# Kernel optimization log

Measured on AMD Instinct MI355X. Metric: run time of the kernel, lower is better.

The kernel has to match this reference:

```python
import jax, jax.numpy as jnp
import numpy as np

N_NODES = 100000
N_EDGES = 6400000
N_TYPES = 16
A1, A2, A3 = 5e-06, 0.0005, 1e-08


def setup_inputs() -> dict:
    key = jax.random.key(0)
    k1, k2, k3, k4, k5, k6 = jax.random.split(key, 6)
    pos = jax.random.normal(k1, (N_NODES, 2), dtype=jnp.float32)
    vel = jax.random.normal(k2, (N_NODES, 2), dtype=jnp.float32)
    p_table = jax.random.uniform(k3, (N_TYPES, 3), dtype=jnp.float32, minval=0.5, maxval=2.0)
    field = jnp.ones((N_NODES, 1), dtype=jnp.float32)
    particle_type = jax.random.randint(k4, (N_NODES,), 0, N_TYPES, dtype=jnp.int32)
    # edges without self-loops (remove_self_loops already applied)
    dst = jax.random.randint(k5, (N_EDGES,), 0, N_NODES, dtype=jnp.int32)
    off = jax.random.randint(k6, (N_EDGES,), 1, N_NODES, dtype=jnp.int32)
    src = (dst + off) % N_NODES
    edge_index = jnp.stack([dst, src], axis=0)  # [2, E], row0=dst(i), row1=src(j)
    return {"pos": pos, "vel": vel, "p_table": p_table, "field": field,
            "particle_type": particle_type, "edge_index": edge_index}


def reference(pos, vel, p_table, field, particle_type, edge_index):
    dst = edge_index[0]  # receiver i
    src = edge_index[1]  # sender j
    dp = pos[src] - pos[dst]            # bc_dpos(pos_j - pos_i), identity BC  [E,2]
    dv = vel[src] - vel[dst]            # d_pos_j - d_pos_i                   [E,2]
    params = p_table[particle_type[dst]]  # parameters_i                      [E,3]
    d2 = jnp.sum(dp * dp, axis=1, keepdims=True)  # [E,1]
    safe_d2 = jnp.where(d2 > 0, d2, 1.0)
    cohesion = params[:, 0:1] * A1 * dp
    alignment = params[:, 1:2] * A2 * dv
    separation = -params[:, 2:3] * A3 * dp / safe_d2
    msg = (separation + alignment + cohesion) * field[src]  # [E,2]
    dd_pos = jax.ops.segment_sum(msg, dst, num_segments=pos.shape[0])  # [N,2]
    return dd_pos
```

## Files before the change

### kernel.cpp

```cpp
#include <hip/hip_runtime.h>
#include <hip/hip_fp16.h>


#define BA1 5e-06f
#define BA2 0.0005f
#define BA3 1e-08f

#define NT 256
#define NTS 1024
#define NWAVE 4
#define SEPB 8192
#define WIN 256
#define WSH 8
#define SPLIT 8
#define NBMAX 512
#define CAP 28672u
#define FPS 4194304.f

__global__ void __launch_bounds__(NT)
k_pack(const float* __restrict__ pos, const float* __restrict__ vel,
       const float* __restrict__ field,
       int N, int NB, int PBLK,
       float4* __restrict__ rec16, unsigned* __restrict__ cursor) {
    int bx = blockIdx.x, tid = threadIdx.x;
    if (bx == PBLK) {
        for (int b = tid; b < NB; b += NT) cursor[b] = (unsigned)b * CAP;
        return;
    }
    int i = bx * NT + tid;
    if (i >= N) return;
    float2 p = *reinterpret_cast<const float2*>(pos + 2 * i);
    float2 v = *reinterpret_cast<const float2*>(vel + 2 * i);
    unsigned short sx = __half_as_ushort(__float2half(v.x));
    unsigned short sy = __half_as_ushort(__float2half(v.y));
    unsigned pv = (unsigned)sx | ((unsigned)sy << 16);
    rec16[i] = make_float4(p.x, p.y, __uint_as_float(pv), field[i]);
}

__global__ void __launch_bounds__(NTS)
k_scatter(const int* __restrict__ dst, const int* __restrict__ src,
          int E, int NB,
          unsigned* __restrict__ cursor,
          unsigned* __restrict__ pk) {
    __shared__ unsigned lh[NBMAX];
    __shared__ unsigned lofs[NBMAX];
    __shared__ unsigned lcur[NBMAX];
    __shared__ unsigned gbase[NBMAX];
    __shared__ unsigned sbuf[SEPB];
    __shared__ unsigned short sbkt[SEPB];
    int blk = blockIdx.x, tid = threadIdx.x;
    int s = blk * SEPB, e = min(E, s + SEPB);

    for (int b = tid; b < NBMAX; b += NTS) lh[b] = 0u;
    __syncthreads();

    int k = s + 4 * tid;
    for (; k + 3 < e; k += 4 * NTS) {
        int4 d = *reinterpret_cast<const int4*>(dst + k);
        atomicAdd(&lh[d.x >> WSH], 1u);
        atomicAdd(&lh[d.y >> WSH], 1u);
        atomicAdd(&lh[d.z >> WSH], 1u);
        atomicAdd(&lh[d.w >> WSH], 1u);
    }
    {
        int rem = (e - s) & 3;
        if (tid < rem) atomicAdd(&lh[dst[e - rem + tid] >> WSH], 1u);
    }
    __syncthreads();
    for (int b = tid; b < NBMAX; b += NTS) lofs[b] = lh[b];
    __syncthreads();

    for (int o = 1; o < NBMAX; o <<= 1) {
        unsigned v0 = 0u, v1 = 0u;
        if (tid < 256) {
            v0 = (tid >= o) ? lh[tid - o] : 0u;
            v1 = (tid + 256 >= o) ? lh[tid + 256 - o] : 0u;
        }
        __syncthreads();
        if (tid < 256) {
            lh[tid] += v0;
            lh[tid + 256] += v1;
        }
        __syncthreads();
    }
    for (int b = tid; b < NBMAX; b += NTS) {
        unsigned c = lofs[b];
        unsigned ex = lh[b] - c;
        lofs[b] = ex;
        lcur[b] = ex;
        if (b < NB && c > 0u) gbase[b] = atomicAdd(&cursor[b], c);
    }
    __syncthreads();

    k = s + 4 * tid;
    for (; k + 3 < e; k += 4 * NTS) {
        int4 d = *reinterpret_cast<const int4*>(dst + k);
        int4 j = *reinterpret_cast<const int4*>(src + k);
        int b0 = d.x >> WSH; unsigned r0 = atomicAdd(&lcur[b0], 1u);
        sbuf[r0] = ((unsigned)(d.x & (WIN - 1)) << 24) | (unsigned)j.x; sbkt[r0] = (unsigned short)b0;
        int b1 = d.y >> WSH; unsigned r1 = atomicAdd(&lcur[b1], 1u);
        sbuf[r1] = ((unsigned)(d.y & (WIN - 1)) << 24) | (unsigned)j.y; sbkt[r1] = (unsigned short)b1;
        int b2 = d.z >> WSH; unsigned r2 = atomicAdd(&lcur[b2], 1u);
        sbuf[r2] = ((unsigned)(d.z & (WIN - 1)) << 24) | (unsigned)j.z; sbkt[r2] = (unsigned short)b2;
        int b3 = d.w >> WSH; unsigned r3 = atomicAdd(&lcur[b3], 1u);
        sbuf[r3] = ((unsigned)(d.w & (WIN - 1)) << 24) | (unsigned)j.w; sbkt[r3] = (unsigned short)b3;
    }
    {
        int rem = (e - s) & 3;
        if (tid < rem) {
            int kk = e - rem + tid;
            int d = dst[kk];
            int b = d >> WSH; unsigned r = atomicAdd(&lcur[b], 1u);
            sbuf[r] = ((unsigned)(d & (WIN - 1)) << 24) | (unsigned)src[kk]; sbkt[r] = (unsigned short)b;
        }
    }
    __syncthreads();

    int ne = e - s;
    for (int t = tid; t < ne; t += NTS) {
        unsigned b = sbkt[t];
        unsigned idx = gbase[b] + ((unsigned)t - lofs[b]);
        if (idx < (b + 1u) * CAP)
            pk[idx] = sbuf[t];
    }
}

__global__ void __launch_bounds__(NT, 4)
k_accum(const float4* __restrict__ rec16,
        const float* __restrict__ p_table,
        const int* __restrict__ ptype,
        const unsigned* __restrict__ pk,
        const unsigned* __restrict__ cursor,
        int N,
        float* __restrict__ out) {
    __shared__ float4 wnode[WIN];
    __shared__ float4 wcoef[WIN];
    __shared__ unsigned long long acc64[NWAVE][WIN];
    int b = blockIdx.x, tid = threadIdx.x;
    int bb = b << WSH;
    int wn = min(N - bb, WIN);
    int wv = tid >> 6;

    if (tid < wn) {
        int g = bb + tid;
        float4 r = rec16[g];
        unsigned u = __float_as_uint(r.z);
        float vx = __half2float(__ushort_as_half((unsigned short)(u & 0xFFFFu)));
        float vy = __half2float(__ushort_as_half((unsigned short)(u >> 16)));
        wnode[tid] = make_float4(r.x, r.y, vx, vy);
        int ty = ptype[g];
        wcoef[tid] = make_float4(p_table[3 * ty + 0] * BA1,
                                 p_table[3 * ty + 1] * BA2,
                                 p_table[3 * ty + 2] * BA3, 0.f);
    }
    {
        unsigned long long* a = &acc64[0][0];
        for (int t = tid; t < NWAVE * WIN; t += NT) a[t] = 0ull;
    }
    __syncthreads();

    unsigned s = (unsigned)b * CAP;
    unsigned c = cursor[b] - s;
    c = (c > CAP) ? CAP : c;
    unsigned e = s + c;

#define EDGE1(PV)                                                              \
    {                                                                          \
        unsigned p_ = (PV);                                                    \
        int l_ = (int)(p_ >> 24);                                              \
        int j_ = (int)(p_ & 0xFFFFFFu);                                        \
        float4 nj_ = rec16[j_];                                                \
        unsigned u_ = __float_as_uint(nj_.z);                                  \
        float vjx_ = __half2float(__ushort_as_half((unsigned short)(u_ & 0xFFFFu))); \
        float vjy_ = __half2float(__ushort_as_half((unsigned short)(u_ >> 16))); \
        float4 w_ = wnode[l_];                                                 \
        float4 c_ = wcoef[l_];                                                 \
        float dpx_ = nj_.x - w_.x, dpy_ = nj_.y - w_.y;                        \
        float dvx_ = vjx_ - w_.z, dvy_ = vjy_ - w_.w;                          \
        float d2_ = dpx_ * dpx_ + dpy_ * dpy_;                                 \
        float sd2_ = (d2_ > 0.f) ? d2_ : 1.f;                                  \
        float cdp_ = c_.x - c_.z / sd2_;                                       \
        float mx_ = (cdp_ * dpx_ + c_.y * dvx_) * nj_.w;                       \
        float my_ = (cdp_ * dpy_ + c_.y * dvy_) * nj_.w;                       \
        long long ax_ = (long long)(int)(mx_ * FPS);                           \
        long long ay_ = (long long)(int)(my_ * FPS);                           \
        atomicAdd(&acc64[wv][l_], (unsigned long long)((ax_ << 32) + ay_));    \
    }

    unsigned stride = (unsigned)NT * SPLIT * 4u;
    for (unsigned k0 = s + ((unsigned)blockIdx.y * NT + tid) * 4u;
         k0 + 4u <= e; k0 += stride) {
        uint4 a = *reinterpret_cast<const uint4*>(pk + k0);
        EDGE1(a.x); EDGE1(a.y); EDGE1(a.z); EDGE1(a.w);
    }
    unsigned tail = c & 3u;
    if (blockIdx.y == 0 && tid < (int)tail) EDGE1(pk[e - tail + tid]);
#undef EDGE1

    __syncthreads();
    for (int l = tid; l < wn; l += NT) {
        unsigned long long T = acc64[0][l] + acc64[1][l] +
                               acc64[2][l] + acc64[3][l];
        long long Ts = (long long)T;
        int yb = (int)(unsigned)(T & 0xFFFFFFFFull);
        long long rem = Ts - (long long)yb;
        int xb = (int)(rem >> 32);
        atomicAdd(&out[2 * (bb + l) + 0], (float)xb * (1.f / FPS));
        atomicAdd(&out[2 * (bb + l) + 1], (float)yb * (1.f / FPS));
    }
}

__global__ void boids_edge_kernel(const float* __restrict__ pos,
                                  const float* __restrict__ vel,
                                  const float* __restrict__ p_table,
                                  const float* __restrict__ field,
                                  const int* __restrict__ ptype,
                                  const int* __restrict__ dst_idx,
                                  const int* __restrict__ src_idx,
                                  float* __restrict__ out,
                                  int n_edges) {
    int e = blockIdx.x * blockDim.x + threadIdx.x;
    if (e >= n_edges) return;
    int i = dst_idx[e], j = src_idx[e];
    float2 pi = *reinterpret_cast<const float2*>(pos + 2 * i);
    float2 pj = *reinterpret_cast<const float2*>(pos + 2 * j);
    float2 vi = *reinterpret_cast<const float2*>(vel + 2 * i);
    float2 vj = *reinterpret_cast<const float2*>(vel + 2 * j);
    float dpx = pj.x - pi.x, dpy = pj.y - pi.y;
    float dvx = vj.x - vi.x, dvy = vj.y - vi.y;
    int t = ptype[i];
    float p0 = p_table[3 * t + 0], p1 = p_table[3 * t + 1], p2 = p_table[3 * t + 2];
    float d2 = dpx * dpx + dpy * dpy;
    float sd2 = (d2 > 0.0f) ? d2 : 1.0f;
    float cdp = p0 * BA1 - p2 * BA3 / sd2;
    float cdv = p1 * BA2;
    float f = field[j];
    atomicAdd(&out[2 * i + 0], (cdp * dpx + cdv * dvx) * f);
    atomicAdd(&out[2 * i + 1], (cdp * dpy + cdv * dvy) * f);
}

extern "C" void kernel_launch(void* const* d_in, const int* in_sizes, int n_in,
                              void* d_out, int out_size, void* d_ws, size_t ws_size,
                              hipStream_t stream) {
    const float* pos     = (const float*)d_in[0];
    const float* vel     = (const float*)d_in[1];
    const float* p_table = (const float*)d_in[2];
    const float* field   = (const float*)d_in[3];
    const int*   ptype   = (const int*)d_in[4];
    const int*   eidx    = (const int*)d_in[5];

    int N = in_sizes[0] / 2;
    int E = in_sizes[5] / 2;
    const int* dstI = eidx;
    const int* srcI = eidx + E;
    float* out = (float*)d_out;

    int NB    = (N + WIN - 1) >> WSH;
    int NSBLK = (E + SEPB - 1) / SEPB;
    int PBLK  = (N + NT - 1) / NT;

    size_t off_rec = 0;
    size_t off_pk  = off_rec + (size_t)N * sizeof(float4);
    size_t off_cur = off_pk + (size_t)NB * CAP * 4;
    size_t need    = off_cur + (size_t)NB * 4;

    bool ok = (ws_size >= need) && (NB <= NBMAX) && (N <= (1 << 24)) &&
              ((E & 3) == 0) &&
              ((size_t)(E / (NB > 0 ? NB : 1)) * 3 / 2 + 64 <= CAP);

    if (!ok) {
        hipMemsetAsync(out, 0, (size_t)out_size * sizeof(float), stream);
        int grid = (E + NT - 1) / NT;
        boids_edge_kernel<<<grid, NT, 0, stream>>>(pos, vel, p_table, field,
                                                   ptype, dstI, srcI, out, E);
        return;
    }

    float4*   rec16  = (float4*)((char*)d_ws + off_rec);
    unsigned* pk     = (unsigned*)((char*)d_ws + off_pk);
    unsigned* cursor = (unsigned*)((char*)d_ws + off_cur);

    hipMemsetAsync(out, 0, (size_t)out_size * sizeof(float), stream);

    k_pack   <<<PBLK + 1, NT, 0, stream>>>(pos, vel, field, N, NB, PBLK,
                                           rec16, cursor);
    k_scatter<<<NSBLK, NTS, 0, stream>>>(dstI, srcI, E, NB, cursor, pk);
    dim3 agrid(NB, SPLIT);
    k_accum  <<<agrid, NT, 0, stream>>>(rec16, p_table, ptype, pk, cursor,
                                        N, out);
}
```

Before: 79.88 us.

## Double destination window to 512 nodes and simplify bucket scatter scan

Destination windows grow from 256 to 512 nodes, which halves the bucket count to 196 and gives each accumulation block about twice as many edges. The local-index field in the packed edge word grows to 9 bits, leaving 23 bits for the source index. The scatter kernel processes larger chunks, drops the separate offset array by folding the exclusive offset into the global base, and uses byte-sized bucket tags to save LDS. The accumulate kernel raises its occupancy hint to 5, but its shared accumulators also double. Fewer, larger blocks may reduce per-block overhead and global cursor atomics, at the cost of lower parallelism and more LDS per block.

```diff
diff --git a/kernel.cpp b/kernel.cpp
--- a/kernel.cpp
+++ b/kernel.cpp
@@ -9,12 +9,12 @@
 #define NT 256
 #define NTS 1024
 #define NWAVE 4
-#define SEPB 8192
-#define WIN 256
-#define WSH 8
-#define SPLIT 8
-#define NBMAX 512
-#define CAP 28672u
+#define SEPB 12288
+#define WIN 512
+#define WSH 9
+#define SPLIT 16
+#define NBMAX 256
+#define CAP 49152u
 #define FPS 4194304.f
 
 __global__ void __launch_bounds__(NT)
@@ -43,15 +43,14 @@
           unsigned* __restrict__ cursor,
           unsigned* __restrict__ pk) {
     __shared__ unsigned lh[NBMAX];
-    __shared__ unsigned lofs[NBMAX];
     __shared__ unsigned lcur[NBMAX];
     __shared__ unsigned gbase[NBMAX];
     __shared__ unsigned sbuf[SEPB];
-    __shared__ unsigned short sbkt[SEPB];
+    __shared__ unsigned char sbkt[SEPB];
     int blk = blockIdx.x, tid = threadIdx.x;
     int s = blk * SEPB, e = min(E, s + SEPB);
 
-    for (int b = tid; b < NBMAX; b += NTS) lh[b] = 0u;
+    if (tid < NBMAX) lh[tid] = 0u;
     __syncthreads();
 
     int k = s + 4 * tid;
@@ -67,28 +66,23 @@
         if (tid < rem) atomicAdd(&lh[dst[e - rem + tid] >> WSH], 1u);
     }
     __syncthreads();
-    for (int b = tid; b < NBMAX; b += NTS) lofs[b] = lh[b];
-    __syncthreads();
 
     for (int o = 1; o < NBMAX; o <<= 1) {
-        unsigned v0 = 0u, v1 = 0u;
-        if (tid < 256) {
-            v0 = (tid >= o) ? lh[tid - o] : 0u;
-            v1 = (tid + 256 >= o) ? lh[tid + 256 - o] : 0u;
+        unsigned v0 = 0u;
+        if (tid < NBMAX && tid >= o) v0 = lh[tid - o];
+        __syncthreads();
+        if (tid < NBMAX) lh[tid] += v0;
+        __syncthreads();
+    }
+    if (tid < NBMAX) {
+        unsigned inc = lh[tid];
+        unsigned ex = (tid > 0) ? lh[tid - 1] : 0u;
+        unsigned c = inc - ex;
+        lcur[tid] = ex;
+        if (tid < NB && c > 0u) {
+            unsigned g = atomicAdd(&cursor[tid], c);
+            gbase[tid] = g - ex;
         }
-        __syncthreads();
-        if (tid < 256) {
-            lh[tid] += v0;
-            lh[tid + 256] += v1;
-        }
-        __syncthreads();
-    }
-    for (int b = tid; b < NBMAX; b += NTS) {
-        unsigned c = lofs[b];
-        unsigned ex = lh[b] - c;
-        lofs[b] = ex;
-        lcur[b] = ex;
-        if (b < NB && c > 0u) gbase[b] = atomicAdd(&cursor[b], c);
     }
     __syncthreads();
 
@@ -97,13 +91,13 @@
         int4 d = *reinterpret_cast<const int4*>(dst + k);
         int4 j = *reinterpret_cast<const int4*>(src + k);
         int b0 = d.x >> WSH; unsigned r0 = atomicAdd(&lcur[b0], 1u);
-        sbuf[r0] = ((unsigned)(d.x & (WIN - 1)) << 24) | (unsigned)j.x; sbkt[r0] = (unsigned short)b0;
+        sbuf[r0] = ((unsigned)(d.x & (WIN - 1)) << 23) | (unsigned)j.x; sbkt[r0] = (unsigned char)b0;
         int b1 = d.y >> WSH; unsigned r1 = atomicAdd(&lcur[b1], 1u);
-        sbuf[r1] = ((unsigned)(d.y & (WIN - 1)) << 24) | (unsigned)j.y; sbkt[r1] = (unsigned short)b1;
+        sbuf[r1] = ((unsigned)(d.y & (WIN - 1)) << 23) | (unsigned)j.y; sbkt[r1] = (unsigned char)b1;
         int b2 = d.z >> WSH; unsigned r2 = atomicAdd(&lcur[b2], 1u);
-        sbuf[r2] = ((unsigned)(d.z & (WIN - 1)) << 24) | (unsigned)j.z; sbkt[r2] = (unsigned short)b2;
+        sbuf[r2] = ((unsigned)(d.z & (WIN - 1)) << 23) | (unsigned)j.z; sbkt[r2] = (unsigned char)b2;
         int b3 = d.w >> WSH; unsigned r3 = atomicAdd(&lcur[b3], 1u);
-        sbuf[r3] = ((unsigned)(d.w & (WIN - 1)) << 24) | (unsigned)j.w; sbkt[r3] = (unsigned short)b3;
+        sbuf[r3] = ((unsigned)(d.w & (WIN - 1)) << 23) | (unsigned)j.w; sbkt[r3] = (unsigned char)b3;
     }
     {
         int rem = (e - s) & 3;
@@ -111,7 +105,7 @@
             int kk = e - rem + tid;
             int d = dst[kk];
             int b = d >> WSH; unsigned r = atomicAdd(&lcur[b], 1u);
-            sbuf[r] = ((unsigned)(d & (WIN - 1)) << 24) | (unsigned)src[kk]; sbkt[r] = (unsigned short)b;
+            sbuf[r] = ((unsigned)(d & (WIN - 1)) << 23) | (unsigned)src[kk]; sbkt[r] = (unsigned char)b;
         }
     }
     __syncthreads();
@@ -119,13 +113,13 @@
     int ne = e - s;
     for (int t = tid; t < ne; t += NTS) {
         unsigned b = sbkt[t];
-        unsigned idx = gbase[b] + ((unsigned)t - lofs[b]);
+        unsigned idx = gbase[b] + (unsigned)t;
         if (idx < (b + 1u) * CAP)
             pk[idx] = sbuf[t];
     }
 }
 
-__global__ void __launch_bounds__(NT, 4)
+__global__ void __launch_bounds__(NT, 5)
 k_accum(const float4* __restrict__ rec16,
         const float* __restrict__ p_table,
         const int* __restrict__ ptype,
@@ -141,17 +135,17 @@
     int wn = min(N - bb, WIN);
     int wv = tid >> 6;
 
-    if (tid < wn) {
-        int g = bb + tid;
+    for (int t = tid; t < wn; t += NT) {
+        int g = bb + t;
         float4 r = rec16[g];
         unsigned u = __float_as_uint(r.z);
         float vx = __half2float(__ushort_as_half((unsigned short)(u & 0xFFFFu)));
         float vy = __half2float(__ushort_as_half((unsigned short)(u >> 16)));
-        wnode[tid] = make_float4(r.x, r.y, vx, vy);
+        wnode[t] = make_float4(r.x, r.y, vx, vy);
         int ty = ptype[g];
-        wcoef[tid] = make_float4(p_table[3 * ty + 0] * BA1,
-                                 p_table[3 * ty + 1] * BA2,
-                                 p_table[3 * ty + 2] * BA3, 0.f);
+        wcoef[t] = make_float4(p_table[3 * ty + 0] * BA1,
+                               p_table[3 * ty + 1] * BA2,
+                               p_table[3 * ty + 2] * BA3, 0.f);
     }
     {
         unsigned long long* a = &acc64[0][0];
@@ -167,8 +161,8 @@
 #define EDGE1(PV)                                                              \
     {                                                                          \
         unsigned p_ = (PV);                                                    \
-        int l_ = (int)(p_ >> 24);                                              \
-        int j_ = (int)(p_ & 0xFFFFFFu);                                        \
+        int l_ = (int)(p_ >> 23);                                              \
+        int j_ = (int)(p_ & 0x7FFFFFu);                                        \
         float4 nj_ = rec16[j_];                                                \
         unsigned u_ = __float_as_uint(nj_.z);                                  \
         float vjx_ = __half2float(__ushort_as_half((unsigned short)(u_ & 0xFFFFu))); \
@@ -264,7 +258,7 @@
     size_t off_cur = off_pk + (size_t)NB * CAP * 4;
     size_t need    = off_cur + (size_t)NB * 4;
 
-    bool ok = (ws_size >= need) && (NB <= NBMAX) && (N <= (1 << 24)) &&
+    bool ok = (ws_size >= need) && (NB <= NBMAX) && (N <= (1 << 23)) &&
               ((E & 3) == 0) &&
               ((size_t)(E / (NB > 0 ? NB : 1)) * 3 / 2 + 64 <= CAP);
 
```

After: 86.52 us. +8.3%, slower.
